# Optimization experiments

Measured on AMD Instinct MI355X. Metric: run time of the kernel, lower is better.

Reference implementation:

```python
import jax, jax.numpy as jnp
import numpy as np

N_NODES = 32768
N_EDGES = 262144
HEAD = 8
CHANNEL = 64
LAYER_NUM = 2
HC = HEAD * CHANNEL  # 512


def setup_inputs() -> dict:
    key = jax.random.key(0)
    ks = jax.random.split(key, 12)
    def lin(k, fan_in, fan_out):
        s = 1.0 / np.sqrt(fan_in)
        kw, kb = jax.random.split(k)
        W = jax.random.uniform(kw, (fan_in, fan_out), jnp.float32, -s, s)
        b = jax.random.uniform(kb, (fan_out,), jnp.float32, -s, s)
        return W, b
    Wn, bn = lin(ks[0], 118, HC)
    We, be = lin(ks[1], 22, HC)
    Wa, ba = lin(ks[2], 2 * HC, HC)
    attn_w = jax.random.normal(ks[3], (1, HEAD, CHANNEL), jnp.float32) * 0.1
    x = jax.random.normal(ks[4], (N_NODES, 118), jnp.float32)
    edge_feat = jax.random.normal(ks[5], (N_EDGES, 22), jnp.float32)
    src = jax.random.randint(ks[6], (N_EDGES,), 0, N_NODES)
    dst = jax.random.randint(ks[7], (N_EDGES,), 0, N_NODES)
    return {"x": x, "edge_feat": edge_feat, "src": src, "dst": dst,
            "Wn": Wn, "bn": bn, "We": We, "be": be, "Wa": Wa, "ba": ba,
            "attn_w": attn_w}


def reference(x, edge_feat, src, dst, Wn, bn, We, be, Wa, ba, attn_w):
    N = x.shape[0]
    H, C = attn_w.shape[1], attn_w.shape[2]
    h = x @ Wn + bn                      # [N, H*C]
    _eh = edge_feat @ We + be            # computed in original forward, never used
    for _ in range(LAYER_NUM):
        # gather src/dst node states onto edges and score them (GATv2 style)
        e = jnp.concatenate([h[src], h[dst]], axis=-1)            # [E, 2HC]
        e = jax.nn.leaky_relu(e @ Wa + ba, negative_slope=0.01)   # [E, HC]
        score = jnp.sum(e.reshape(-1, H, C) * attn_w, axis=-1)    # [E, H]
        # edge softmax normalized over incoming edges of each dst node
        m = jax.ops.segment_max(score, dst, num_segments=N)       # [N, H]
        ex = jnp.exp(score - m[dst])                              # [E, H]
        denom = jax.ops.segment_sum(ex, dst, num_segments=N)      # [N, H]
        alpha = ex / denom[dst]                                   # [E, H]
        # weighted message passing: u_mul_e then sum over dst
        msg = h[src].reshape(-1, H, C) * alpha[:, :, None]        # [E, H, C]
        h = jax.ops.segment_sum(msg, dst, num_segments=N).reshape(N, H * C)
    return h
```

## Files before the change

kernel.cpp:

```cpp
#include <hip/hip_runtime.h>
#include <hip/hip_bf16.h>
#include <stdint.h>

#define N_NODES 32768
#define N_EDGES 262144

typedef __attribute__((ext_vector_type(8))) short short8;
typedef __attribute__((ext_vector_type(4))) float f32x4;

__device__ __forceinline__ float bf2f(ushort u) {
  return __uint_as_float(((uint)u) << 16);
}
__device__ __forceinline__ ushort f2bf(float f) {
  uint x = __float_as_uint(f);
  uint r = (x + 0x7fffu + ((x >> 16) & 1u)) >> 16;
  return (ushort)r;
}
__device__ __forceinline__ float loadf(const void* p, size_t i, int isbf) {
  return isbf ? bf2f(((const ushort*)p)[i]) : ((const float*)p)[i];
}

__global__ void detect_dtype(const uint* __restrict__ xw, int* __restrict__ flag) {
  __shared__ int cnt;
  if (threadIdx.x == 0) cnt = 0;
  __syncthreads();
  int good = 0;
  for (int i = threadIdx.x; i < 1024; i += 256) {
    uint lo = xw[i] & 0xFFFFu;
    uint ef = (lo >> 7) & 0xFFu;
    if (lo == 0u || (ef >= 0x60u && ef <= 0x90u)) good++;
  }
  atomicAdd(&cnt, good);
  __syncthreads();
  if (threadIdx.x == 0) *flag = (cnt >= 614) ? 1 : 0;
}

__global__ void setup_small(const void* __restrict__ ba, const void* __restrict__ bn,
                            const void* __restrict__ aw, const int* __restrict__ flag,
                            float* __restrict__ bias2, float* __restrict__ bnf,
                            float* __restrict__ wf) {
  int fl = *flag;
  int t = blockIdx.x * blockDim.x + threadIdx.x;
  if (t < 1024) bias2[t] = (t < 512) ? loadf(ba, t, fl) : 0.f;
  if (t < 512) { bnf[t] = loadf(bn, t, fl); wf[t] = loadf(aw, t, fl); }
}

__global__ void build_wnt(const void* __restrict__ Wn, const int* __restrict__ flag,
                          ushort* __restrict__ WnpT) {
  int fl = *flag;
  int t = blockIdx.x * blockDim.x + threadIdx.x;
  int n = t >> 7, k = t & 127;
  WnpT[t] = (k < 118) ? f2bf(loadf(Wn, (size_t)k * 512 + n, fl)) : (ushort)0;
}

__global__ void build_xp(const void* __restrict__ x, const int* __restrict__ flag,
                         ushort* __restrict__ xp) {
  int fl = *flag;
  int t = blockIdx.x * blockDim.x + threadIdx.x;
  int i = t >> 7, k = t & 127;
  xp[t] = (k < 118) ? f2bf(loadf(x, (size_t)i * 118 + k, fl)) : (ushort)0;
}

__global__ void build_w2t(const void* __restrict__ Wa, const int* __restrict__ flag,
                          ushort* __restrict__ W2T) {
  int fl = *flag;
  int t = blockIdx.x * blockDim.x + threadIdx.x;
  int n = t >> 9, k = t & 511;
  size_t idx = (n < 512) ? ((size_t)k * 512 + n) : ((size_t)(512 + k) * 512 + (n - 512));
  W2T[t] = f2bf(loadf(Wa, idx, fl));
}

__global__ void csr_count(const int* __restrict__ dst, int* __restrict__ cnt) {
  int e = blockIdx.x * blockDim.x + threadIdx.x;
  atomicAdd(&cnt[dst[e]], 1);
}

__global__ __launch_bounds__(1024)
void csr_scan(const int* __restrict__ cnt, int* __restrict__ rowptr,
              int* __restrict__ cursor) {
  __shared__ int part[1024];
  const int t = threadIdx.x;
  const int base = t * 32;
  int loc[32];
  int s = 0;
#pragma unroll
  for (int i = 0; i < 32; ++i) { loc[i] = s; s += cnt[base + i]; }
  part[t] = s;
  __syncthreads();
  for (int off = 1; off < 1024; off <<= 1) {
    int v = (t >= off) ? part[t - off] : 0;
    __syncthreads();
    part[t] += v;
    __syncthreads();
  }
  int pre = (t == 0) ? 0 : part[t - 1];
#pragma unroll
  for (int i = 0; i < 32; ++i) {
    int v = pre + loc[i];
    rowptr[base + i] = v;
    cursor[base + i] = v;
  }
  if (t == 1023) rowptr[N_NODES] = part[1023];
}

__global__ void csr_fill(const int* __restrict__ dst, int* __restrict__ cursor,
                         int* __restrict__ eidx) {
  int e = blockIdx.x * blockDim.x + threadIdx.x;
  int p = atomicAdd(&cursor[dst[e]], 1);
  eidx[p] = e;
}

__global__ __launch_bounds__(256)
void gemm_bf16(const ushort* __restrict__ A, const ushort* __restrict__ BT,
               const float* __restrict__ bias, ushort* __restrict__ C,
               int M, int N, int K) {
  __shared__ __align__(16) ushort As[128 * 32];
  __shared__ __align__(16) ushort Bs[128 * 32];
  const int tid = threadIdx.x, wave = tid >> 6, lane = tid & 63;
  const int bm = blockIdx.y * 128, bn = blockIdx.x * 128;
  const int wm = (wave >> 1) * 64, wn = (wave & 1) * 64;
  const int fcol = lane & 15, quad = lane >> 4;

  const f32x4 zero = {0.f, 0.f, 0.f, 0.f};
  f32x4 acc[4][4];
#pragma unroll
  for (int i = 0; i < 4; ++i)
#pragma unroll
    for (int j = 0; j < 4; ++j) acc[i][j] = zero;

  for (int k0 = 0; k0 < K; k0 += 32) {
#pragma unroll
    for (int r = 0; r < 2; ++r) {
      int o = r * 4096 + wave * 1024 + lane * 16;
      int row = o >> 6;
      int ke = (o & 63) >> 1;
      short8 va = *(const short8*)(A + (size_t)(bm + row) * K + k0 + ke);
      short8 vb = *(const short8*)(BT + (size_t)(bn + row) * K + k0 + ke);
      *(short8*)&As[o >> 1] = va;
      *(short8*)&Bs[o >> 1] = vb;
    }
    __syncthreads();
    short8 a[4], b[4];
#pragma unroll
    for (int i = 0; i < 4; ++i) {
      a[i] = *(const short8*)&As[(wm + i * 16 + fcol) * 32 + quad * 8];
      b[i] = *(const short8*)&Bs[(wn + i * 16 + fcol) * 32 + quad * 8];
    }
#pragma unroll
    for (int i = 0; i < 4; ++i)
#pragma unroll
      for (int j = 0; j < 4; ++j)
        acc[i][j] = __builtin_amdgcn_mfma_f32_16x16x32_bf16(a[i], b[j], acc[i][j], 0, 0, 0);
    __syncthreads();
  }

#pragma unroll
  for (int i = 0; i < 4; ++i) {
    int rowb = bm + wm + i * 16 + quad * 4;
#pragma unroll
    for (int j = 0; j < 4; ++j) {
      int col = bn + wn + j * 16 + fcol;
      float bb = bias[col];
#pragma unroll
      for (int r = 0; r < 4; ++r) {
        C[(size_t)(rowb + r) * N + col] = f2bf(acc[i][j][r] + bb);
      }
    }
  }
}

__global__ __launch_bounds__(256)
void node_fused(const ushort* __restrict__ PQ, const ushort* __restrict__ hb_in,
                const int* __restrict__ src, const int* __restrict__ eidx,
                const int* __restrict__ rowptr, const float* __restrict__ wf,
                const int* __restrict__ flag, ushort* __restrict__ hb_out,
                void* __restrict__ out, int write_out) {
  const int wave = threadIdx.x >> 6, lane = threadIdx.x & 63;
  const int d = blockIdx.x * 4 + wave;
  const int beg = rowptr[d], end = rowptr[d + 1];
  const int c0 = lane * 8;

  const uint4 qv = *(const uint4*)(PQ + (size_t)d * 1024 + 512 + c0);
  const uint qw[4] = {qv.x, qv.y, qv.z, qv.w};
  float q[8], w[8];
#pragma unroll
  for (int i = 0; i < 4; ++i) {
    q[2 * i]     = __uint_as_float(qw[i] << 16);
    q[2 * i + 1] = __uint_as_float(qw[i] & 0xffff0000u);
  }
  const float4 w0 = *(const float4*)(wf + c0);
  const float4 w1 = *(const float4*)(wf + c0 + 4);
  w[0] = w0.x; w[1] = w0.y; w[2] = w0.z; w[3] = w0.w;
  w[4] = w1.x; w[5] = w1.y; w[6] = w1.z; w[7] = w1.w;

  float m = -3e38f, den = 0.f;
  float acc[8] = {0.f, 0.f, 0.f, 0.f, 0.f, 0.f, 0.f, 0.f};

  int sj = (beg < end) ? src[eidx[beg]] : 0;
  for (int j = beg; j < end; ++j) {
    const int s = sj;
    if (j + 1 < end) sj = src[eidx[j + 1]];
    const uint4 pv = *(const uint4*)(PQ + (size_t)s * 1024 + c0);
    const uint4 hv = *(const uint4*)(hb_in + (size_t)s * 512 + c0);
    const uint pw[4] = {pv.x, pv.y, pv.z, pv.w};
    const uint hw[4] = {hv.x, hv.y, hv.z, hv.w};
    float t = 0.f;
#pragma unroll
    for (int i = 0; i < 4; ++i) {
      float ea = __uint_as_float(pw[i] << 16) + q[2 * i];
      float eb = __uint_as_float(pw[i] & 0xffff0000u) + q[2 * i + 1];
      ea = (ea > 0.f) ? ea : 0.01f * ea;
      eb = (eb > 0.f) ? eb : 0.01f * eb;
      t += ea * w[2 * i] + eb * w[2 * i + 1];
    }
    t += __shfl_xor(t, 1);
    t += __shfl_xor(t, 2);
    t += __shfl_xor(t, 4);
    const float mnew = fmaxf(m, t);
    const float corr = __expf(m - mnew);
    const float ex = __expf(t - mnew);
    den = den * corr + ex;
#pragma unroll
    for (int i = 0; i < 4; ++i) {
      acc[2 * i]     = acc[2 * i] * corr     + ex * __uint_as_float(hw[i] << 16);
      acc[2 * i + 1] = acc[2 * i + 1] * corr + ex * __uint_as_float(hw[i] & 0xffff0000u);
    }
    m = mnew;
  }

  const float inv = (end > beg) ? (1.f / den) : 0.f;
  uint o[4];
#pragma unroll
  for (int i = 0; i < 4; ++i) {
    float v0 = acc[2 * i] * inv, v1 = acc[2 * i + 1] * inv;
    o[i] = (uint)f2bf(v0) | ((uint)f2bf(v1) << 16);
  }
  *(uint4*)(hb_out + (size_t)d * 512 + c0) = *(uint4*)o;
  if (write_out) {
    if (*flag) {
      *(uint4*)((ushort*)out + (size_t)d * 512 + c0) = *(uint4*)o;
    } else {
      float4 f0 = {acc[0] * inv, acc[1] * inv, acc[2] * inv, acc[3] * inv};
      float4 f1 = {acc[4] * inv, acc[5] * inv, acc[6] * inv, acc[7] * inv};
      *(float4*)((float*)out + (size_t)d * 512 + c0) = f0;
      *(float4*)((float*)out + (size_t)d * 512 + c0 + 4) = f1;
    }
  }
}

extern "C" void kernel_launch(void* const* d_in, const int* in_sizes, int n_in,
                              void* d_out, int out_size, void* d_ws, size_t ws_size,
                              hipStream_t stream) {
  const void* x   = d_in[0];
  const int*  src = (const int*)d_in[2];
  const int*  dst = (const int*)d_in[3];
  const void* Wn  = d_in[4];
  const void* bn  = d_in[5];
  const void* Wa  = d_in[8];
  const void* ba  = d_in[9];
  const void* aw  = d_in[10];

  char* ws = (char*)d_ws;
  size_t off = 0;
  auto alloc = [&](size_t bytes) {
    char* p = ws + off;
    off = (off + bytes + 255) & ~(size_t)255;
    return p;
  };
  ushort* hbA    = (ushort*)alloc((size_t)N_NODES * 512 * 2);
  ushort* hbB    = (ushort*)alloc((size_t)N_NODES * 512 * 2);
  ushort* PQ     = (ushort*)alloc((size_t)N_NODES * 1024 * 2);
  int*    eidx   = (int*)   alloc((size_t)N_EDGES * 4);
  int*    rowptr = (int*)   alloc((size_t)(N_NODES + 1) * 4);
  int*    cnt    = (int*)   alloc((size_t)N_NODES * 4);
  int*    cursor = (int*)   alloc((size_t)N_NODES * 4);
  ushort* W2T    = (ushort*)alloc((size_t)1024 * 512 * 2);
  float*  bias2  = (float*) alloc(1024 * 4);
  ushort* xp     = (ushort*)alloc((size_t)N_NODES * 128 * 2);
  ushort* WnpT   = (ushort*)alloc((size_t)512 * 128 * 2);
  float*  bnf    = (float*) alloc(512 * 4);
  float*  wf     = (float*) alloc(512 * 4);
  int*    flag   = (int*)   alloc(256);

  detect_dtype<<<1, 256, 0, stream>>>((const uint*)x, flag);
  setup_small<<<4, 256, 0, stream>>>(ba, bn, aw, flag, bias2, bnf, wf);
  build_wnt<<<(512 * 128) / 256, 256, 0, stream>>>(Wn, flag, WnpT);
  build_xp<<<(N_NODES * 128) / 256, 256, 0, stream>>>(x, flag, xp);
  build_w2t<<<(1024 * 512) / 256, 256, 0, stream>>>(Wa, flag, W2T);

  hipMemsetAsync(cnt, 0, (size_t)N_NODES * 4, stream);
  csr_count<<<N_EDGES / 256, 256, 0, stream>>>(dst, cnt);
  csr_scan<<<1, 1024, 0, stream>>>(cnt, rowptr, cursor);
  csr_fill<<<N_EDGES / 256, 256, 0, stream>>>(dst, cursor, eidx);

  {
    dim3 g(512 / 128, N_NODES / 128);
    gemm_bf16<<<g, 256, 0, stream>>>(xp, WnpT, bnf, hbA, N_NODES, 512, 128);
  }

  ushort* hin = hbA;
  ushort* hout = hbB;
  for (int layer = 0; layer < 2; ++layer) {
    dim3 g(1024 / 128, N_NODES / 128);
    gemm_bf16<<<g, 256, 0, stream>>>(hin, W2T, bias2, PQ, N_NODES, 1024, 512);
    node_fused<<<N_NODES / 4, 256, 0, stream>>>(PQ, hin, src, eidx, rowptr, wf, flag,
                                                hout, d_out, layer == 1 ? 1 : 0);
    ushort* t = hin; hin = hout; hout = t;
  }
}
```

Before: 493.0 us.

## Merge weight-prep kernels and load GEMM tiles directly into LDS

Three small weight-preparation kernels are merged into a single launch that dispatches on block index, removing two kernel launches. The GEMM tile staging now uses global_load_lds, which copies global memory straight into shared memory and skips the round trip through registers. The direct-to-LDS path assumes that each lane's 16-byte destination follows wave-contiguous ordering, which the existing layout (lane*16 offset) satisfies. It needs 16-byte global_load_lds support on the target.

```diff
diff --git a/kernel.cpp b/kernel.cpp
--- a/kernel.cpp
+++ b/kernel.cpp
@@ -7,6 +7,9 @@
 
 typedef __attribute__((ext_vector_type(8))) short short8;
 typedef __attribute__((ext_vector_type(4))) float f32x4;
+
+typedef const __attribute__((address_space(1))) void* gvp;
+typedef __attribute__((address_space(3))) void* lvp;
 
 __device__ __forceinline__ float bf2f(ushort u) {
   return __uint_as_float(((uint)u) << 16);
@@ -35,22 +38,28 @@
   if (threadIdx.x == 0) *flag = (cnt >= 614) ? 1 : 0;
 }
 
-__global__ void setup_small(const void* __restrict__ ba, const void* __restrict__ bn,
-                            const void* __restrict__ aw, const int* __restrict__ flag,
-                            float* __restrict__ bias2, float* __restrict__ bnf,
-                            float* __restrict__ wf) {
-  int fl = *flag;
-  int t = blockIdx.x * blockDim.x + threadIdx.x;
-  if (t < 1024) bias2[t] = (t < 512) ? loadf(ba, t, fl) : 0.f;
-  if (t < 512) { bnf[t] = loadf(bn, t, fl); wf[t] = loadf(aw, t, fl); }
-}
-
-__global__ void build_wnt(const void* __restrict__ Wn, const int* __restrict__ flag,
-                          ushort* __restrict__ WnpT) {
-  int fl = *flag;
-  int t = blockIdx.x * blockDim.x + threadIdx.x;
-  int n = t >> 7, k = t & 127;
-  WnpT[t] = (k < 118) ? f2bf(loadf(Wn, (size_t)k * 512 + n, fl)) : (ushort)0;
+__global__ void prep_weights(const void* __restrict__ Wa, const void* __restrict__ Wn,
+                             const void* __restrict__ ba, const void* __restrict__ bn,
+                             const void* __restrict__ aw, const int* __restrict__ flag,
+                             ushort* __restrict__ W2T, ushort* __restrict__ WnpT,
+                             float* __restrict__ bias2, float* __restrict__ bnf,
+                             float* __restrict__ wf) {
+  const int fl = *flag;
+  const int b = blockIdx.x;
+  if (b < 2048) {
+    int t = b * 256 + threadIdx.x;
+    int n = t >> 9, k = t & 511;
+    size_t idx = (n < 512) ? ((size_t)k * 512 + n) : ((size_t)(512 + k) * 512 + (n - 512));
+    W2T[t] = f2bf(loadf(Wa, idx, fl));
+  } else if (b < 2304) {
+    int t = (b - 2048) * 256 + threadIdx.x;
+    int n = t >> 7, k = t & 127;
+    WnpT[t] = (k < 118) ? f2bf(loadf(Wn, (size_t)k * 512 + n, fl)) : (ushort)0;
+  } else {
+    int t = (b - 2304) * 256 + threadIdx.x;
+    if (t < 1024) bias2[t] = (t < 512) ? loadf(ba, t, fl) : 0.f;
+    if (t < 512) { bnf[t] = loadf(bn, t, fl); wf[t] = loadf(aw, t, fl); }
+  }
 }
 
 __global__ void build_xp(const void* __restrict__ x, const int* __restrict__ flag,
@@ -59,15 +68,6 @@
   int t = blockIdx.x * blockDim.x + threadIdx.x;
   int i = t >> 7, k = t & 127;
   xp[t] = (k < 118) ? f2bf(loadf(x, (size_t)i * 118 + k, fl)) : (ushort)0;
-}
-
-__global__ void build_w2t(const void* __restrict__ Wa, const int* __restrict__ flag,
-                          ushort* __restrict__ W2T) {
-  int fl = *flag;
-  int t = blockIdx.x * blockDim.x + threadIdx.x;
-  int n = t >> 9, k = t & 511;
-  size_t idx = (n < 512) ? ((size_t)k * 512 + n) : ((size_t)(512 + k) * 512 + (n - 512));
-  W2T[t] = f2bf(loadf(Wa, idx, fl));
 }
 
 __global__ void csr_count(const int* __restrict__ dst, int* __restrict__ cnt) {
@@ -134,10 +134,12 @@
       int o = r * 4096 + wave * 1024 + lane * 16;
       int row = o >> 6;
       int ke = (o & 63) >> 1;
-      short8 va = *(const short8*)(A + (size_t)(bm + row) * K + k0 + ke);
-      short8 vb = *(const short8*)(BT + (size_t)(bn + row) * K + k0 + ke);
-      *(short8*)&As[o >> 1] = va;
-      *(short8*)&Bs[o >> 1] = vb;
+      const ushort* gA = A + (size_t)(bm + row) * K + k0 + ke;
+      const ushort* gB = BT + (size_t)(bn + row) * K + k0 + ke;
+      ushort* lA = As + ((r * 4096 + wave * 1024) >> 1);
+      ushort* lB = Bs + ((r * 4096 + wave * 1024) >> 1);
+      __builtin_amdgcn_global_load_lds((gvp)(const void*)gA, (lvp)(void*)lA, 16, 0, 0);
+      __builtin_amdgcn_global_load_lds((gvp)(const void*)gB, (lvp)(void*)lB, 16, 0, 0);
     }
     __syncthreads();
     short8 a[4], b[4];
@@ -283,10 +285,9 @@
   int*    flag   = (int*)   alloc(256);
 
   detect_dtype<<<1, 256, 0, stream>>>((const uint*)x, flag);
-  setup_small<<<4, 256, 0, stream>>>(ba, bn, aw, flag, bias2, bnf, wf);
-  build_wnt<<<(512 * 128) / 256, 256, 0, stream>>>(Wn, flag, WnpT);
+  prep_weights<<<2308, 256, 0, stream>>>(Wa, Wn, ba, bn, aw, flag,
+                                         W2T, WnpT, bias2, bnf, wf);
   build_xp<<<(N_NODES * 128) / 256, 256, 0, stream>>>(x, flag, xp);
-  build_w2t<<<(1024 * 512) / 256, 256, 0, stream>>>(Wa, flag, W2T);
 
   hipMemsetAsync(cnt, 0, (size_t)N_NODES * 4, stream);
   csr_count<<<N_EDGES / 256, 256, 0, stream>>>(dst, cnt);
```

Result: no change. 486.0 us (-1.4%).
